# Performance work log

Measured on AMD Instinct MI355X. Metric: run time of the kernel, lower is better.

The kernel has to match this reference:

```python
import jax, jax.numpy as jnp
import numpy as np

VMF_KAPPA = 30.0      # vMF concentration
THRESHOLD = 0.0       # vc_thresholds
OCC_LIKELY = 0.6      # occ_likely[0]
NUM_MIXTURES = 4
EPS_L1 = 1e-12        # torch F.normalize eps


def _l1_normalize(x, axis):
    n = jnp.sum(jnp.abs(x), axis=axis, keepdims=True)
    return x / jnp.maximum(n, EPS_L1)


def _crop_or_pad(mm, H, W):
    # center crop or zero-pad mix model spatial dims to (H, W); shapes are static
    _, _, hm, wm = mm.shape
    if hm < H:
        d1 = (H - hm) // 2
        mm = jnp.pad(mm, ((0, 0), (0, 0), (d1, H - hm - d1), (0, 0)))
    elif hm > H:
        d1 = (hm - H) // 2
        mm = mm[:, :, d1:d1 + H, :]
    if wm < W:
        d1 = (W - wm) // 2
        mm = jnp.pad(mm, ((0, 0), (0, 0), (0, 0), (d1, W - wm - d1)))
    elif wm > W:
        d1 = (wm - W) // 2
        mm = mm[:, :, :, d1:d1 + W]
    return mm


def setup_inputs() -> dict:
    key = jax.random.key(0)
    k1, k2, k3, k4 = jax.random.split(key, 4)
    B, C, H, W = 32, 512, 56, 56
    VC = 512              # number of vMF codebook vectors
    KM = 48               # num_classes(12) * num_mixtures(4)
    NCLUT = 5             # clutter models
    return {
        "vgg_feat": jax.random.normal(k1, (B, C, H, W), dtype=jnp.float32),
        "conv_weight": jax.random.normal(k2, (VC, C, 1, 1), dtype=jnp.float32),
        "mix_model": jax.random.uniform(k3, (KM, VC, H, W), dtype=jnp.float32),
        "clutter_model": jax.random.uniform(k4, (NCLUT, VC), dtype=jnp.float32),
    }


def reference(vgg_feat, conv_weight, mix_model, clutter_model):
    B, C, H, W = vgg_feat.shape
    # --- Conv1o1: cosine similarity between L2-normalized features and codebook ---
    xnorm = jnp.linalg.norm(vgg_feat, axis=1, keepdims=True)
    xnorm = xnorm + (xnorm == 0).astype(vgg_feat.dtype)  # avoid div-by-zero
    xn = vgg_feat / xnorm
    w = conv_weight[:, :, 0, 0]                           # (vc, C) 1x1 kernel
    wn = w / jnp.linalg.norm(w, axis=1, keepdims=True)
    cos = jnp.einsum('bchw,kc->bkhw', xn, wn)             # (B, vc, H, W)
    # --- vMF activation ---
    act = jnp.exp(VMF_KAPPA * cos) * (cos > THRESHOLD).astype(cos.dtype)
    # --- PointwiseInferenceLayer (vmf, use_mixture_bg=True) ---
    ck = _l1_normalize(jnp.clip(clutter_model, 0.0, 1.0), axis=1)  # (N, vc)
    bg = jnp.einsum('bkhw,nk->bnhw', act, ck)                      # (B, N, H, W)
    background = jnp.log(bg * OCC_LIKELY + 1e-10)
    background = jnp.max(background, axis=1, keepdims=True)        # (B, 1, H, W)
    background = background[:, None, None]                         # (B,1,1,1,H,W)

    mm = _l1_normalize(jnp.clip(mix_model, 0.0, 1.0), axis=1)      # (KM, vc, Hm, Wm)
    mm = _crop_or_pad(mm, H, W)
    fg = jnp.einsum('bkhw,mkhw->bmhw', act, mm)                    # (B, KM, H, W)
    foreground = jnp.log(fg * (1.0 - OCC_LIKELY) + 1e-10)
    num_classes = mm.shape[0] // NUM_MIXTURES
    foreground = foreground.reshape(B, num_classes, NUM_MIXTURES, 1, H, W)
    per_model = jnp.maximum(foreground, background).sum(axis=(-1, -2))  # (B,K,M,1)
    scores = per_model.max(axis=-1).max(axis=-1)                        # (B, K)
    mix_likeli = scores / (H * W)
    # SoftMaxTemp(2.0)
    z = jnp.exp(jnp.clip(mix_likeli * 2.0, -88.7, 88.7))
    soft = z / jnp.sum(z, axis=1, keepdims=True)
    return soft, vgg_feat, mix_likeli
```

## Files before the change

### kernel.cpp

```cpp
#include <hip/hip_runtime.h>

#define B_ 32
#define C_ 512
#define HW_ 3136
#define KF_ 512
#define KM_ 48
#define NCL_ 5

typedef __attribute__((ext_vector_type(8))) short short8;
typedef __attribute__((ext_vector_type(4))) short short4v;
typedef __attribute__((ext_vector_type(4))) float floatx4;

__device__ __forceinline__ unsigned short f2bf(float f) {
    union { float f; unsigned u; } v; v.f = f;
    unsigned r = v.u + 0x7FFFu + ((v.u >> 16) & 1u);
    return (unsigned short)(r >> 16);
}
__device__ __forceinline__ float bf2f(unsigned short u) {
    union { unsigned u; float f; } v; v.u = ((unsigned)u) << 16;
    return v.f;
}

__global__ __launch_bounds__(64) void prep_kernel(const float* __restrict__ w,
                                                  const float* __restrict__ cl,
                                                  unsigned short* __restrict__ wn,
                                                  float* __restrict__ ck) {
    int bid = blockIdx.x, t = threadIdx.x;
    if (bid < KF_) {
        const float* row = w + (size_t)bid * C_;
        float ss = 0.f;
        float x[8];
#pragma unroll
        for (int j = 0; j < 8; ++j) { x[j] = row[t * 8 + j]; ss += x[j] * x[j]; }
        for (int m = 32; m >= 1; m >>= 1) ss += __shfl_xor(ss, m);
        float inv = 1.f / sqrtf(ss);
#pragma unroll
        for (int j = 0; j < 8; ++j) wn[(size_t)bid * C_ + t * 8 + j] = f2bf(x[j] * inv);
    } else {
        int n = bid - KF_;
        if (n >= NCL_) return;
        const float* row = cl + (size_t)n * KF_;
        float s = 0.f;
        float v[8];
#pragma unroll
        for (int j = 0; j < 8; ++j) {
            float x = row[t * 8 + j];
            x = fminf(fmaxf(x, 0.f), 1.f);
            v[j] = x; s += x;
        }
        for (int m = 32; m >= 1; m >>= 1) s += __shfl_xor(s, m);
        float inv = 1.f / fmaxf(s, 1e-12f);
#pragma unroll
        for (int j = 0; j < 8; ++j) ck[(size_t)n * KF_ + t * 8 + j] = v[j] * inv;
    }
}

__global__ __launch_bounds__(512, 4) void cosact_kernel(const float* __restrict__ vgg,
                                                        const unsigned short* __restrict__ wn,
                                                        unsigned short* __restrict__ act,
                                                        float* __restrict__ out_vgg,
                                                        int write_vgg) {
    int ht = blockIdx.x, b = blockIdx.y;
    int tid = threadIdx.x;
    int lane = tid & 63, wid = tid >> 6;
    int wr = wid & 1, wc = wid >> 1;

    __shared__ __align__(16) unsigned short xn[64 * 520];
    __shared__ __align__(16) unsigned short wnl[64 * 72];
    __shared__ float ssp[8][64];
    __shared__ float inv_s[64];

    int px = tid & 63;
    int cq = tid >> 6;
    const float* vcol = vgg + (size_t)b * C_ * HW_ + (size_t)ht * 64 + px;
    float* ovcol = out_vgg + (size_t)b * C_ * HW_ + (size_t)ht * 64 + px;

    float ss = 0.f;
#pragma unroll
    for (int j = 0; j < 16; ++j) {
        int c0 = cq * 64 + j * 4;
        float x0 = vcol[(size_t)(c0 + 0) * HW_];
        float x1 = vcol[(size_t)(c0 + 1) * HW_];
        float x2 = vcol[(size_t)(c0 + 2) * HW_];
        float x3 = vcol[(size_t)(c0 + 3) * HW_];
        ss += x0 * x0 + x1 * x1 + x2 * x2 + x3 * x3;
        short4v pk;
        pk[0] = (short)f2bf(x0); pk[1] = (short)f2bf(x1);
        pk[2] = (short)f2bf(x2); pk[3] = (short)f2bf(x3);
        *(short4v*)&xn[px * 520 + c0] = pk;
        if (write_vgg) {
            ovcol[(size_t)(c0 + 0) * HW_] = x0;
            ovcol[(size_t)(c0 + 1) * HW_] = x1;
            ovcol[(size_t)(c0 + 2) * HW_] = x2;
            ovcol[(size_t)(c0 + 3) * HW_] = x3;
        }
    }
    ssp[cq][px] = ss;
    __syncthreads();
    if (tid < 64) {
        float s = 0.f;
#pragma unroll
        for (int q = 0; q < 8; ++q) s += ssp[q][tid];
        float n = sqrtf(s);
        inv_s[tid] = (n == 0.f) ? 1.f : 1.f / n;
    }
    __syncthreads();

    int pxc = wc * 16 + (lane & 15);
    float inv_px = inv_s[pxc];

    int wk = tid >> 3, wcg = tid & 7;
    short8 wreg = *(const short8*)(wn + (size_t)wk * C_ + wcg * 8);

    unsigned short* actp = act + ((size_t)b * HW_ + (size_t)ht * 64 + pxc) * KF_;

    for (int kt = 0; kt < 8; ++kt) {
        floatx4 acc0 = {}, acc1 = {};
        for (int ct = 0; ct < 8; ++ct) {
            __syncthreads();
            *(short8*)&wnl[wk * 72 + wcg * 8] = wreg;
            int nct = ct + 1, nkt = kt;
            if (nct == 8) { nct = 0; nkt = kt + 1; }
            if (nkt < 8)
                wreg = *(const short8*)(wn + (size_t)(nkt * 64 + wk) * C_ + nct * 64 + wcg * 8);
            __syncthreads();
#pragma unroll
            for (int ks = 0; ks < 2; ++ks) {
                short8 bfr = *(const short8*)&xn[pxc * 520 + ct * 64 + ks * 32 + (lane >> 4) * 8];
                short8 af0 = *(const short8*)&wnl[(wr * 32 + 0 + (lane & 15)) * 72 + ks * 32 + (lane >> 4) * 8];
                short8 af1 = *(const short8*)&wnl[(wr * 32 + 16 + (lane & 15)) * 72 + ks * 32 + (lane >> 4) * 8];
                acc0 = __builtin_amdgcn_mfma_f32_16x16x32_bf16(af0, bfr, acc0, 0, 0, 0);
                acc1 = __builtin_amdgcn_mfma_f32_16x16x32_bf16(af1, bfr, acc1, 0, 0, 0);
            }
        }
#pragma unroll
        for (int mi = 0; mi < 2; ++mi) {
            floatx4 a = mi ? acc1 : acc0;
            short4v pk;
#pragma unroll
            for (int r = 0; r < 4; ++r) {
                float cv = a[r] * inv_px;
                float av = cv > 0.f ? expf(30.f * cv) : 0.f;
                pk[r] = (short)f2bf(av);
            }
            int kbase = kt * 64 + wr * 32 + mi * 16 + (lane >> 4) * 4;
            *(short4v*)(actp + kbase) = pk;
        }
    }
}

__global__ __launch_bounds__(256) void bg_kernel(const unsigned short* __restrict__ act,
                                                 const float* __restrict__ ck,
                                                 float* __restrict__ bgout) {
    __shared__ float ckl[NCL_ * KF_];
    int tid = threadIdx.x;
    for (int i = tid; i < NCL_ * KF_; i += 256) ckl[i] = ck[i];
    __syncthreads();
    int p = blockIdx.x * 256 + tid;
    int b = blockIdx.y;
    if (p >= HW_) return;
    const unsigned short* row = act + ((size_t)b * HW_ + p) * KF_;
    float acc[NCL_] = {0.f, 0.f, 0.f, 0.f, 0.f};
    for (int k8 = 0; k8 < KF_ / 8; ++k8) {
        short8 v = *(const short8*)(row + k8 * 8);
#pragma unroll
        for (int j = 0; j < 8; ++j) {
            float a = bf2f((unsigned short)v[j]);
#pragma unroll
            for (int n = 0; n < NCL_; ++n) acc[n] += a * ckl[n * KF_ + k8 * 8 + j];
        }
    }
    float m = -1e30f;
#pragma unroll
    for (int n = 0; n < NCL_; ++n) m = fmaxf(m, logf(acc[n] * 0.6f + 1e-10f));
    bgout[(size_t)b * HW_ + p] = m;
}

__global__ __launch_bounds__(512, 4) void fg_kernel(const unsigned short* __restrict__ act,
                                                    const float* __restrict__ mm,
                                                    const float* __restrict__ bgin,
                                                    float* __restrict__ pm) {
    int p0 = blockIdx.x * 16;
    int mt = blockIdx.y;
    int tid = threadIdx.x;
    int lane = tid & 63, wid = tid >> 6;

    __shared__ __align__(16) unsigned short actl[4 * 4224];
    __shared__ __align__(16) unsigned short mml[4 * 2176];
    __shared__ float csum_s[16 * 16];
    __shared__ float pms[16 * 32];
    __shared__ float bgs[32 * 16];

    if (tid < 256) csum_s[tid] = 0.f;
    pms[tid] = 0.f;
    {
        int bb = tid >> 4, pp = tid & 15;
        bgs[tid] = bgin[(size_t)bb * HW_ + p0 + pp];
    }

    int akg = tid & 3, ap = (tid >> 2) & 15, ab0 = tid >> 6;
    int mmm = tid >> 5, mkq = (tid >> 2) & 7, mpq = tid & 3;
    const unsigned short* abase = act + ((size_t)0 * HW_) ;
    const float* mbase = mm + ((size_t)(mt * 16 + mmm) * KF_ + mkq * 4) * HW_ + p0 + mpq * 4;

    const short8* fA[2];
    const short8* fB[2][2];
#pragma unroll
    for (int e = 0; e < 2; ++e) {
        int pp = wid * 2 + e;
        fA[e] = (const short8*)&mml[(lane >> 4) * 2176 + pp * 136 + (lane & 15) * 8];
#pragma unroll
        for (int bf = 0; bf < 2; ++bf)
            fB[e][bf] = (const short8*)&actl[(lane >> 4) * 4224 + pp * 264 + (bf * 16 + (lane & 15)) * 8];
    }

    floatx4 acc[2][2] = {};
    float csr[4] = {};

    short8 areg[4];
    floatx4 mreg[4];
#pragma unroll
    for (int j = 0; j < 4; ++j)
        areg[j] = *(const short8*)(act + ((size_t)(ab0 + j * 8) * HW_ + p0 + ap) * KF_ + akg * 8);
#pragma unroll
    for (int kk = 0; kk < 4; ++kk)
        mreg[kk] = *(const floatx4*)(mbase + (size_t)kk * HW_);

    for (int ch = 0; ch < 16; ++ch) {
        __syncthreads();
#pragma unroll
        for (int j = 0; j < 4; ++j)
            *(short8*)&actl[akg * 4224 + ap * 264 + (ab0 + j * 8) * 8] = areg[j];
#pragma unroll
        for (int i = 0; i < 4; ++i) {
            float c0 = fminf(fmaxf(mreg[0][i], 0.f), 1.f);
            float c1 = fminf(fmaxf(mreg[1][i], 0.f), 1.f);
            float c2 = fminf(fmaxf(mreg[2][i], 0.f), 1.f);
            float c3 = fminf(fmaxf(mreg[3][i], 0.f), 1.f);
            csr[i] += c0 + c1 + c2 + c3;
            short4v pk;
            pk[0] = (short)f2bf(c0); pk[1] = (short)f2bf(c1);
            pk[2] = (short)f2bf(c2); pk[3] = (short)f2bf(c3);
            *(short4v*)&mml[(mkq >> 1) * 2176 + (mpq * 4 + i) * 136 + mmm * 8 + (mkq & 1) * 4] = pk;
        }
        if (ch < 15) {
            int k0 = (ch + 1) * 32;
#pragma unroll
            for (int j = 0; j < 4; ++j)
                areg[j] = *(const short8*)(act + ((size_t)(ab0 + j * 8) * HW_ + p0 + ap) * KF_ + k0 + akg * 8);
#pragma unroll
            for (int kk = 0; kk < 4; ++kk)
                mreg[kk] = *(const floatx4*)(mbase + (size_t)(k0 + kk) * HW_);
        }
        __syncthreads();
#pragma unroll
        for (int e = 0; e < 2; ++e) {
            short8 af = *fA[e];
            short8 b0 = *fB[e][0];
            short8 b1 = *fB[e][1];
            acc[e][0] = __builtin_amdgcn_mfma_f32_16x16x32_bf16(af, b0, acc[e][0], 0, 0, 0);
            acc[e][1] = __builtin_amdgcn_mfma_f32_16x16x32_bf16(af, b1, acc[e][1], 0, 0, 0);
        }
    }

#pragma unroll
    for (int i = 0; i < 4; ++i)
        atomicAdd(&csum_s[mmm * 16 + mpq * 4 + i], csr[i]);
    __syncthreads();

#pragma unroll
    for (int e = 0; e < 2; ++e) {
        int pp = wid * 2 + e;
#pragma unroll
        for (int bf = 0; bf < 2; ++bf) {
            int bcol = bf * 16 + (lane & 15);
            float bgv = bgs[bcol * 16 + pp];
#pragma unroll
            for (int r = 0; r < 4; ++r) {
                int m = (lane >> 4) * 4 + r;
                float invn = 1.f / fmaxf(csum_s[m * 16 + pp], 1e-12f);
                float v = fmaxf(logf(acc[e][bf][r] * invn * 0.4f + 1e-10f), bgv);
                atomicAdd(&pms[m * 32 + bcol], v);
            }
        }
    }
    __syncthreads();
    {
        int m = tid >> 5, bcol = tid & 31;
        atomicAdd(&pm[(size_t)bcol * KM_ + mt * 16 + m], pms[m * 32 + bcol]);
    }
}

__global__ __launch_bounds__(64) void final_kernel(const float* __restrict__ pm,
                                                   float* __restrict__ out_soft,
                                                   float* __restrict__ out_ml) {
    int b = threadIdx.x;
    if (b >= B_) return;
    float ml[12];
#pragma unroll
    for (int c = 0; c < 12; ++c) {
        float s = -1e30f;
#pragma unroll
        for (int j = 0; j < 4; ++j) s = fmaxf(s, pm[(size_t)b * KM_ + c * 4 + j]);
        ml[c] = s / (float)HW_;
    }
    float z[12], zs = 0.f;
#pragma unroll
    for (int c = 0; c < 12; ++c) {
        float e = fminf(fmaxf(ml[c] * 2.f, -88.7f), 88.7f);
        z[c] = expf(e); zs += z[c];
    }
#pragma unroll
    for (int c = 0; c < 12; ++c) {
        out_soft[(size_t)b * 12 + c] = z[c] / zs;
        out_ml[(size_t)b * 12 + c] = ml[c];
    }
}

extern "C" void kernel_launch(void* const* d_in, const int* in_sizes, int n_in,
                              void* d_out, int out_size, void* d_ws, size_t ws_size,
                              hipStream_t stream) {
    const float* vgg = (const float*)d_in[0];
    const float* cw  = (const float*)d_in[1];
    const float* mmp = (const float*)d_in[2];
    const float* cl  = (const float*)d_in[3];
    float* out = (float*)d_out;
    char* ws = (char*)d_ws;

    unsigned short* wn = (unsigned short*)(ws);
    float* ck          = (float*)(ws + 524288);
    float* bg          = (float*)(ws + 534528);
    float* pm          = (float*)(ws + 935936);
    const size_t ACT_OFF = 942080;
    const size_t ACT_BYTES = (size_t)B_ * HW_ * KF_ * 2;

    int big_ws = (ws_size >= ACT_OFF + ACT_BYTES) ? 1 : 0;
    unsigned short* act = big_ws ? (unsigned short*)(ws + ACT_OFF)
                                 : (unsigned short*)(out + 384);

    hipMemsetAsync(pm, 0, (size_t)B_ * KM_ * sizeof(float), stream);
    prep_kernel<<<dim3(KF_ + NCL_), dim3(64), 0, stream>>>(cw, cl, wn, ck);
    cosact_kernel<<<dim3(49, 32), dim3(512), 0, stream>>>(vgg, wn, act, out + 384, big_ws);
    bg_kernel<<<dim3(13, 32), dim3(256), 0, stream>>>(act, ck, bg);
    fg_kernel<<<dim3(196, 3), dim3(512), 0, stream>>>(act, mmp, bg, pm);
    final_kernel<<<1, 64, 0, stream>>>(pm, out, out + 384 + (size_t)B_ * C_ * HW_);
    if (!big_ws)
        hipMemcpyAsync(out + 384, vgg, (size_t)B_ * C_ * HW_ * sizeof(float),
                       hipMemcpyDeviceToDevice, stream);
}
```

Measured before the change: 472.2 us.

## Split cosine GEMM into transpose prep plus tiled MFMA GEMM with fused background

The fused cosact kernel is split in two. A prep kernel writes bf16-transposed normalized features and inverse norms to workspace. A 128x128-tiled MFMA GEMM then loads both operands with global_load_lds and computes the vMF activation. The background clutter dot products are folded into the GEMM epilogue through LDS and global atomics, which removes the separate bg_kernel pass over act. The cost is an extra round trip through a roughly 100MB bf16 transposed buffer, a larger workspace requirement, an extra memset, and atomic accumulation.

```diff
diff --git a/kernel.cpp b/kernel.cpp
--- a/kernel.cpp
+++ b/kernel.cpp
@@ -10,6 +10,9 @@
 typedef __attribute__((ext_vector_type(8))) short short8;
 typedef __attribute__((ext_vector_type(4))) short short4v;
 typedef __attribute__((ext_vector_type(4))) float floatx4;
+typedef unsigned int u32;
+typedef u32 __attribute__((address_space(1))) gu32;
+typedef u32 __attribute__((address_space(3))) lu32;
 
 __device__ __forceinline__ unsigned short f2bf(float f) {
     union { float f; unsigned u; } v; v.f = f;
@@ -19,6 +22,9 @@
 __device__ __forceinline__ float bf2f(unsigned short u) {
     union { unsigned u; float f; } v; v.u = ((unsigned)u) << 16;
     return v.f;
+}
+__device__ __forceinline__ void gl2lds16(const unsigned short* g, unsigned short* l) {
+    __builtin_amdgcn_global_load_lds((const gu32*)g, (lu32*)l, 16, 0, 0);
 }
 
 __global__ __launch_bounds__(64) void prep_kernel(const float* __restrict__ w,
@@ -55,25 +61,18 @@
     }
 }
 
-__global__ __launch_bounds__(512, 4) void cosact_kernel(const float* __restrict__ vgg,
-                                                        const unsigned short* __restrict__ wn,
-                                                        unsigned short* __restrict__ act,
-                                                        float* __restrict__ out_vgg,
-                                                        int write_vgg) {
-    int ht = blockIdx.x, b = blockIdx.y;
+__global__ __launch_bounds__(512) void xprep_kernel(const float* __restrict__ vgg,
+                                                    unsigned short* __restrict__ xnt,
+                                                    float* __restrict__ invn,
+                                                    float* __restrict__ out_vgg,
+                                                    int write_vgg) {
+    int pt = blockIdx.x, b = blockIdx.y;
     int tid = threadIdx.x;
-    int lane = tid & 63, wid = tid >> 6;
-    int wr = wid & 1, wc = wid >> 1;
-
-    __shared__ __align__(16) unsigned short xn[64 * 520];
-    __shared__ __align__(16) unsigned short wnl[64 * 72];
+    int px = tid & 63, cq = tid >> 6;
+    __shared__ __align__(16) unsigned short tile[64][512];
     __shared__ float ssp[8][64];
-    __shared__ float inv_s[64];
-
-    int px = tid & 63;
-    int cq = tid >> 6;
-    const float* vcol = vgg + (size_t)b * C_ * HW_ + (size_t)ht * 64 + px;
-    float* ovcol = out_vgg + (size_t)b * C_ * HW_ + (size_t)ht * 64 + px;
+    const float* vcol = vgg + (size_t)b * C_ * HW_ + pt * 64 + px;
+    float* ovcol = out_vgg + (size_t)b * C_ * HW_ + pt * 64 + px;
 
     float ss = 0.f;
 #pragma unroll
@@ -87,7 +86,7 @@
         short4v pk;
         pk[0] = (short)f2bf(x0); pk[1] = (short)f2bf(x1);
         pk[2] = (short)f2bf(x2); pk[3] = (short)f2bf(x3);
-        *(short4v*)&xn[px * 520 + c0] = pk;
+        *(short4v*)&tile[px][c0] = pk;
         if (write_vgg) {
             ovcol[(size_t)(c0 + 0) * HW_] = x0;
             ovcol[(size_t)(c0 + 1) * HW_] = x1;
@@ -102,83 +101,111 @@
 #pragma unroll
         for (int q = 0; q < 8; ++q) s += ssp[q][tid];
         float n = sqrtf(s);
-        inv_s[tid] = (n == 0.f) ? 1.f : 1.f / n;
-    }
-    __syncthreads();
-
-    int pxc = wc * 16 + (lane & 15);
-    float inv_px = inv_s[pxc];
-
-    int wk = tid >> 3, wcg = tid & 7;
-    short8 wreg = *(const short8*)(wn + (size_t)wk * C_ + wcg * 8);
-
-    unsigned short* actp = act + ((size_t)b * HW_ + (size_t)ht * 64 + pxc) * KF_;
-
-    for (int kt = 0; kt < 8; ++kt) {
-        floatx4 acc0 = {}, acc1 = {};
-        for (int ct = 0; ct < 8; ++ct) {
-            __syncthreads();
-            *(short8*)&wnl[wk * 72 + wcg * 8] = wreg;
-            int nct = ct + 1, nkt = kt;
-            if (nct == 8) { nct = 0; nkt = kt + 1; }
-            if (nkt < 8)
-                wreg = *(const short8*)(wn + (size_t)(nkt * 64 + wk) * C_ + nct * 64 + wcg * 8);
-            __syncthreads();
-#pragma unroll
-            for (int ks = 0; ks < 2; ++ks) {
-                short8 bfr = *(const short8*)&xn[pxc * 520 + ct * 64 + ks * 32 + (lane >> 4) * 8];
-                short8 af0 = *(const short8*)&wnl[(wr * 32 + 0 + (lane & 15)) * 72 + ks * 32 + (lane >> 4) * 8];
-                short8 af1 = *(const short8*)&wnl[(wr * 32 + 16 + (lane & 15)) * 72 + ks * 32 + (lane >> 4) * 8];
-                acc0 = __builtin_amdgcn_mfma_f32_16x16x32_bf16(af0, bfr, acc0, 0, 0, 0);
-                acc1 = __builtin_amdgcn_mfma_f32_16x16x32_bf16(af1, bfr, acc1, 0, 0, 0);
+        invn[(size_t)b * HW_ + pt * 64 + tid] = (n == 0.f) ? 1.f : 1.f / n;
+    }
+    __syncthreads();
+    int row = tid >> 3, ch = tid & 7;
+    unsigned short* orow = xnt + ((size_t)b * HW_ + pt * 64 + row) * 512;
+#pragma unroll
+    for (int j = 0; j < 8; ++j) {
+        int c8 = (ch + 8 * j) * 8;
+        *(short8*)(orow + c8) = *(const short8*)&tile[row][c8];
+    }
+}
+
+__global__ __launch_bounds__(256) void gemm_act_kernel(const unsigned short* __restrict__ xnt,
+                                                       const unsigned short* __restrict__ wn,
+                                                       const float* __restrict__ invn,
+                                                       const float* __restrict__ ck,
+                                                       unsigned short* __restrict__ act,
+                                                       float* __restrict__ bgacc) {
+    int pt = blockIdx.x, ft = blockIdx.y;
+    int tid = threadIdx.x, lane = tid & 63, w = tid >> 6;
+    int wm = w & 1, wq = w >> 1;
+    __shared__ __align__(16) unsigned short a_lds[128 * 64];
+    __shared__ __align__(16) unsigned short b_lds[128 * 64];
+    __shared__ float ck_l[NCL_ * KF_];
+    __shared__ float inv_l[128];
+    __shared__ float bga_l[128 * NCL_];
+
+    for (int i = tid; i < NCL_ * KF_; i += 256) ck_l[i] = ck[i];
+    if (tid < 128) inv_l[tid] = invn[(size_t)pt * 128 + tid];
+    for (int i = tid; i < 128 * NCL_; i += 256) bga_l[i] = 0.f;
+
+    const unsigned short* ga = wn + ((size_t)(ft * 128) + (tid >> 3)) * 512 + (tid & 7) * 8;
+    const unsigned short* gb = xnt + ((size_t)pt * 128 + (tid >> 3)) * 512 + (tid & 7) * 8;
+    unsigned short* la = a_lds + (tid >> 3) * 64 + (tid & 7) * 8;
+    unsigned short* lb = b_lds + (tid >> 3) * 64 + (tid & 7) * 8;
+
+    floatx4 acc[4][4] = {};
+    for (int ks = 0; ks < 8; ++ks) {
+#pragma unroll
+        for (int s = 0; s < 4; ++s) {
+            gl2lds16(ga + (size_t)s * 32 * 512 + ks * 64, la + s * 32 * 64);
+            gl2lds16(gb + (size_t)s * 32 * 512 + ks * 64, lb + s * 32 * 64);
+        }
+        __syncthreads();
+#pragma unroll
+        for (int k2 = 0; k2 < 2; ++k2) {
+            short8 af[4], bf[4];
+#pragma unroll
+            for (int i = 0; i < 4; ++i) {
+                af[i] = *(const short8*)&a_lds[(wm * 64 + i * 16 + (lane & 15)) * 64 + k2 * 32 + (lane >> 4) * 8];
+                bf[i] = *(const short8*)&b_lds[(wq * 64 + i * 16 + (lane & 15)) * 64 + k2 * 32 + (lane >> 4) * 8];
             }
-        }
-#pragma unroll
-        for (int mi = 0; mi < 2; ++mi) {
-            floatx4 a = mi ? acc1 : acc0;
+#pragma unroll
+            for (int mi = 0; mi < 4; ++mi)
+#pragma unroll
+                for (int ni = 0; ni < 4; ++ni)
+                    acc[mi][ni] = __builtin_amdgcn_mfma_f32_16x16x32_bf16(af[mi], bf[ni], acc[mi][ni], 0, 0, 0);
+        }
+        __syncthreads();
+    }
+
+#pragma unroll
+    for (int ni = 0; ni < 4; ++ni) {
+        int px_l = wq * 64 + ni * 16 + (lane & 15);
+        float inv = inv_l[px_l];
+        size_t row_g = (size_t)pt * 128 + px_l;
+        float bp[NCL_] = {0.f, 0.f, 0.f, 0.f, 0.f};
+#pragma unroll
+        for (int mi = 0; mi < 4; ++mi) {
+            int f_g = ft * 128 + wm * 64 + mi * 16 + (lane >> 4) * 4;
             short4v pk;
+            float av[4];
 #pragma unroll
             for (int r = 0; r < 4; ++r) {
-                float cv = a[r] * inv_px;
-                float av = cv > 0.f ? expf(30.f * cv) : 0.f;
-                pk[r] = (short)f2bf(av);
+                float cv = acc[mi][ni][r] * inv;
+                float a = cv > 0.f ? __expf(30.f * cv) : 0.f;
+                av[r] = a;
+                pk[r] = (short)f2bf(a);
             }
-            int kbase = kt * 64 + wr * 32 + mi * 16 + (lane >> 4) * 4;
-            *(short4v*)(actp + kbase) = pk;
-        }
-    }
-}
-
-__global__ __launch_bounds__(256) void bg_kernel(const unsigned short* __restrict__ act,
-                                                 const float* __restrict__ ck,
-                                                 float* __restrict__ bgout) {
-    __shared__ float ckl[NCL_ * KF_];
-    int tid = threadIdx.x;
-    for (int i = tid; i < NCL_ * KF_; i += 256) ckl[i] = ck[i];
-    __syncthreads();
-    int p = blockIdx.x * 256 + tid;
-    int b = blockIdx.y;
-    if (p >= HW_) return;
-    const unsigned short* row = act + ((size_t)b * HW_ + p) * KF_;
-    float acc[NCL_] = {0.f, 0.f, 0.f, 0.f, 0.f};
-    for (int k8 = 0; k8 < KF_ / 8; ++k8) {
-        short8 v = *(const short8*)(row + k8 * 8);
-#pragma unroll
-        for (int j = 0; j < 8; ++j) {
-            float a = bf2f((unsigned short)v[j]);
-#pragma unroll
-            for (int n = 0; n < NCL_; ++n) acc[n] += a * ckl[n * KF_ + k8 * 8 + j];
-        }
-    }
-    float m = -1e30f;
-#pragma unroll
-    for (int n = 0; n < NCL_; ++n) m = fmaxf(m, logf(acc[n] * 0.6f + 1e-10f));
-    bgout[(size_t)b * HW_ + p] = m;
+            *(short4v*)(act + row_g * 512 + f_g) = pk;
+#pragma unroll
+            for (int n = 0; n < NCL_; ++n)
+                bp[n] += av[0] * ck_l[n * KF_ + f_g] + av[1] * ck_l[n * KF_ + f_g + 1] +
+                         av[2] * ck_l[n * KF_ + f_g + 2] + av[3] * ck_l[n * KF_ + f_g + 3];
+        }
+#pragma unroll
+        for (int n = 0; n < NCL_; ++n) {
+            float v = bp[n];
+            v += __shfl_xor(v, 16);
+            v += __shfl_xor(v, 32);
+            if ((lane >> 4) == 0) atomicAdd(&bga_l[px_l * NCL_ + n], v);
+        }
+    }
+    __syncthreads();
+    if (tid < 128) {
+        size_t row_g = (size_t)pt * 128 + tid;
+#pragma unroll
+        for (int n = 0; n < NCL_; ++n)
+            atomicAdd(&bgacc[row_g * 8 + n], bga_l[tid * NCL_ + n]);
+    }
 }
 
 __global__ __launch_bounds__(512, 4) void fg_kernel(const unsigned short* __restrict__ act,
                                                     const float* __restrict__ mm,
-                                                    const float* __restrict__ bgin,
+                                                    const float* __restrict__ bgacc,
                                                     float* __restrict__ pm) {
     int p0 = blockIdx.x * 16;
     int mt = blockIdx.y;
@@ -195,12 +222,15 @@
     pms[tid] = 0.f;
     {
         int bb = tid >> 4, pp = tid & 15;
-        bgs[tid] = bgin[(size_t)bb * HW_ + p0 + pp];
+        const float* bga = bgacc + ((size_t)bb * HW_ + p0 + pp) * 8;
+        float mx = -1e30f;
+#pragma unroll
+        for (int n = 0; n < NCL_; ++n) mx = fmaxf(mx, logf(bga[n] * 0.6f + 1e-10f));
+        bgs[tid] = mx;
     }
 
     int akg = tid & 3, ap = (tid >> 2) & 15, ab0 = tid >> 6;
     int mmm = tid >> 5, mkq = (tid >> 2) & 7, mpq = tid & 3;
-    const unsigned short* abase = act + ((size_t)0 * HW_) ;
     const float* mbase = mm + ((size_t)(mt * 16 + mmm) * KF_ + mkq * 4) * HW_ + p0 + mpq * 4;
 
     const short8* fA[2];
@@ -327,11 +357,13 @@
     float* out = (float*)d_out;
     char* ws = (char*)d_ws;
 
-    unsigned short* wn = (unsigned short*)(ws);
-    float* ck          = (float*)(ws + 524288);
-    float* bg          = (float*)(ws + 534528);
-    float* pm          = (float*)(ws + 935936);
-    const size_t ACT_OFF = 942080;
+    unsigned short* wn   = (unsigned short*)(ws);
+    float* ck            = (float*)(ws + 524288);
+    float* invn          = (float*)(ws + 534528);
+    float* pm            = (float*)(ws + 935936);
+    float* bgacc         = (float*)(ws + 942080);
+    unsigned short* xnt  = (unsigned short*)(ws + 4153344);
+    const size_t ACT_OFF = 4153344 + 102760448;
     const size_t ACT_BYTES = (size_t)B_ * HW_ * KF_ * 2;
 
     int big_ws = (ws_size >= ACT_OFF + ACT_BYTES) ? 1 : 0;
@@ -339,10 +371,11 @@
                                  : (unsigned short*)(out + 384);
 
     hipMemsetAsync(pm, 0, (size_t)B_ * KM_ * sizeof(float), stream);
+    hipMemsetAsync(bgacc, 0, (size_t)B_ * HW_ * 8 * sizeof(float), stream);
     prep_kernel<<<dim3(KF_ + NCL_), dim3(64), 0, stream>>>(cw, cl, wn, ck);
-    cosact_kernel<<<dim3(49, 32), dim3(512), 0, stream>>>(vgg, wn, act, out + 384, big_ws);
-    bg_kernel<<<dim3(13, 32), dim3(256), 0, stream>>>(act, ck, bg);
-    fg_kernel<<<dim3(196, 3), dim3(512), 0, stream>>>(act, mmp, bg, pm);
+    xprep_kernel<<<dim3(49, 32), dim3(512), 0, stream>>>(vgg, xnt, invn, out + 384, big_ws);
+    gemm_act_kernel<<<dim3(784, 4), dim3(256), 0, stream>>>(xnt, wn, invn, ck, act, bgacc);
+    fg_kernel<<<dim3(196, 3), dim3(512), 0, stream>>>(act, mmp, bgacc, pm);
     final_kernel<<<1, 64, 0, stream>>>(pm, out, out + 384 + (size_t)B_ * C_ * HW_);
     if (!big_ws)
         hipMemcpyAsync(out + 384, vgg, (size_t)B_ * C_ * HW_ * sizeof(float),
```

After: 496.4 us. 5.1% more time.
